# Performance work log

Hardware: AMD Instinct MI355X
Metric: run time of the kernel (lower is better)

Reference implementation:

```python
import jax, jax.numpy as jnp
import numpy as np

# Static cluster layout: B graphs, PER atoms each; first NIN are 'inside'
# (aux_ind==0), remaining NOUT are 'outside' periodic images (aux_ind==1).
B, PER, NIN, K = 256, 1024, 256, 32
NOUT = PER - NIN
N = B * PER
R = 6.0        # cutoff radius (Angstrom)
BOX = 32.0     # box side -> ~30 neighbors within R at this density


def setup_inputs() -> dict:
    key = jax.random.key(0)
    pos = jax.random.uniform(key, (N, 3), dtype=jnp.float32) * BOX
    batch = (jnp.arange(N, dtype=jnp.int32) // PER)
    aux_ind = ((jnp.arange(N, dtype=jnp.int32) % PER) >= NIN).astype(jnp.int32)
    return {"pos": pos, "batch": batch, "aux_ind": aux_ind}


def _select_neighbors(d, valid, k):
    """Pick up to k valid candidates per target, lowest candidate index first.
    d: [..., C] distances, valid: [..., C] bool. Returns (idx, mask, dist),
    each [..., k]; padded slots have mask=False and dist=0."""
    C = d.shape[-1]
    order_key = jnp.where(valid, jnp.arange(C, dtype=jnp.int32), C + 1)
    idx = jnp.argsort(order_key, axis=-1)[..., :k]          # [..., k]
    mask = jnp.take_along_axis(valid, idx, axis=-1)
    dist = jnp.where(mask, jnp.take_along_axis(d, idx, axis=-1), 0.0)
    return idx.astype(jnp.int32), mask, dist


def reference(pos, batch, aux_ind):
    # batch/aux_ind are encoded by the static contiguous layout above;
    # they parameterize the same structure torch builds via scatter_add/cumsum.
    pg = pos.reshape(B, PER, 3)
    ins = pg[:, :NIN]            # [B, NIN, 3]  inside (target + intra-conv) nodes
    outs = pg[:, NIN:]           # [B, NOUT, 3] outside (inter-conv) nodes

    # intra edges: inside -> inside, same graph, no self loops
    d_ii = jnp.sqrt(jnp.sum((ins[:, :, None, :] - ins[:, None, :, :]) ** 2, -1))  # [B,NIN,NIN]
    valid_ii = (d_ii < R) & ~jnp.eye(NIN, dtype=bool)
    idx_ii, m_ii, dist_ii = _select_neighbors(d_ii, valid_ii, K)

    # inter edges: outside -> inside, same graph
    d_io = jnp.sqrt(jnp.sum((ins[:, :, None, :] - outs[:, None, :, :]) ** 2, -1))  # [B,NIN,NOUT]
    valid_io = d_io < R
    idx_io, m_io, dist_io = _select_neighbors(d_io, valid_io, K)

    # relabel to global node indices (flow='source_to_target': row=source, col=target)
    goff = (jnp.arange(B, dtype=jnp.int32) * PER)[:, None, None]       # [B,1,1]
    tgt = jnp.broadcast_to(goff + jnp.arange(NIN, dtype=jnp.int32)[None, :, None],
                           (B, NIN, K))
    src_ii = goff + idx_ii
    src_io = goff + NIN + idx_io

    edge_index = jnp.stack([src_ii.reshape(-1), tgt.reshape(-1)], 0)        # [2, B*NIN*K]
    edge_index_inter = jnp.stack([src_io.reshape(-1), tgt.reshape(-1)], 0)  # [2, B*NIN*K]

    return (edge_index, m_ii.reshape(-1), dist_ii,
            edge_index_inter, m_io.reshape(-1), dist_io)
```

## Files before the change

### kernel.cpp

```cpp
#include <hip/hip_runtime.h>


constexpr int KK = 32;
constexpr unsigned EE = 2097152u;

typedef float v2f __attribute__((ext_vector_type(2)));

__device__ __forceinline__ v2f pk_add(v2f a, v2f b) {
    v2f d; asm("v_pk_add_f32 %0, %1, %2" : "=v"(d) : "v"(a), "v"(b)); return d;
}
__device__ __forceinline__ v2f pk_mul(v2f a, v2f b) {
    v2f d; asm("v_pk_mul_f32 %0, %1, %2" : "=v"(d) : "v"(a), "v"(b)); return d;
}

__device__ __forceinline__ int prefix_lt(unsigned long long m) {
    return __builtin_amdgcn_mbcnt_hi((unsigned)(m >> 32),
           __builtin_amdgcn_mbcnt_lo((unsigned)m, 0u));
}

__global__ __launch_bounds__(256) void mo3e_kernel(const float* __restrict__ pos,
                                                   float* __restrict__ out) {
    __shared__ float sq[3072];
    __shared__ int   slotrow[4][128];

    const int blk = blockIdx.x;
    const int b   = blk >> 6;
    const int tid = threadIdx.x;
    const int w   = tid >> 6;
    const int l   = tid & 63;
    const int i   = __builtin_amdgcn_readfirstlane(((blk & 63) << 2) | w);

    {
        const float4* g4 = (const float4*)(pos + (size_t)b * 3072);
        float4* s4 = (float4*)sq;
        s4[tid      ] = g4[tid      ];
        s4[tid + 256] = g4[tid + 256];
        s4[tid + 512] = g4[tid + 512];
    }
    __syncthreads();

    const float xi = sq[3 * i], yi = sq[3 * i + 1], zi = sq[3 * i + 2];
    const v2f nx = {-xi, -xi}, ny = {-yi, -yi}, nz = {-zi, -zi};

    int* __restrict__ row = slotrow[w];
    const int dump = 64 + l;

    unsigned long long msk[16];
    int cii = 0, cio = 0;
    int av = 3 * l;

#pragma unroll
    for (int it = 0; it < 2; ++it) {
        const float xa = sq[av], ya = sq[av + 1], za = sq[av + 2];
        const float xb = sq[av + 192], yb = sq[av + 193], zb = sq[av + 194];
        av += 384;
        const v2f qx = {xa, xb}, qy = {ya, yb}, qz = {za, zb};
        const v2f dx = pk_add(qx, nx), dy = pk_add(qy, ny), dz = pk_add(qz, nz);
        const v2f d2 = pk_add(pk_add(pk_mul(dx, dx), pk_mul(dy, dy)), pk_mul(dz, dz));
        const int c0 = it * 128;
        {
            const bool va = (d2.x < 36.0f) & ((c0 + l) != i);
            const unsigned long long m = __ballot(va);
            msk[2 * it] = m;
            int ent = cii + prefix_lt(m);
            ent = ent < 127 ? ent : 127;
            ent = va ? ent : dump;
            row[ent] = c0 + l;
            cii += __popcll(m);
        }
        {
            const bool vb = (d2.y < 36.0f) & ((c0 + 64 + l) != i);
            const unsigned long long m = __ballot(vb);
            msk[2 * it + 1] = m;
            int ent = cii + prefix_lt(m);
            ent = ent < 127 ? ent : 127;
            ent = vb ? ent : dump;
            row[ent] = c0 + 64 + l;
            cii += __popcll(m);
        }
    }
    const int S0ii = cii < KK ? cii : KK;
    if (cii < KK) {
        int pc = cii;
#pragma unroll
        for (int g = 0; g < 4; ++g) {
            const unsigned long long inv = ~msk[g];
            const bool pm = (inv >> l) & 1ull;
            int ent = pc + prefix_lt(inv);
            ent = pm ? ent : dump;
            row[ent] = g * 64 + l;
            pc += __popcll(inv);
            if (pc >= KK) break;
        }
    }

#pragma unroll
    for (int it = 2; it < 8; ++it) {
        const float xa = sq[av], ya = sq[av + 1], za = sq[av + 2];
        const float xb = sq[av + 192], yb = sq[av + 193], zb = sq[av + 194];
        av += 384;
        const v2f qx = {xa, xb}, qy = {ya, yb}, qz = {za, zb};
        const v2f dx = pk_add(qx, nx), dy = pk_add(qy, ny), dz = pk_add(qz, nz);
        const v2f d2 = pk_add(pk_add(pk_mul(dx, dx), pk_mul(dy, dy)), pk_mul(dz, dz));
        const int c0 = it * 128;
        {
            const bool va = (d2.x < 36.0f);
            const unsigned long long m = __ballot(va);
            msk[2 * it] = m;
            int ent = cio + prefix_lt(m);
            ent = ent < 95 ? ent : 95;
            ent = va ? ent + KK : dump;
            row[ent] = c0 + l;
            cio += __popcll(m);
        }
        {
            const bool vb = (d2.y < 36.0f);
            const unsigned long long m = __ballot(vb);
            msk[2 * it + 1] = m;
            int ent = cio + prefix_lt(m);
            ent = ent < 95 ? ent : 95;
            ent = vb ? ent + KK : dump;
            row[ent] = c0 + 64 + l;
            cio += __popcll(m);
        }
    }
    const int S0io = cio < KK ? cio : KK;
    if (cio < KK) {
        int pc = cio;
#pragma unroll
        for (int g = 4; g < 16; ++g) {
            const unsigned long long inv = ~msk[g];
            const bool pm = (inv >> l) & 1ull;
            int ent = pc + prefix_lt(inv);
            ent = pm ? ent + KK : dump;
            row[ent] = g * 64 + l;
            pc += __popcll(inv);
            if (pc >= KK) break;
        }
    }

    {
        const int idx = row[l];
        const float qx = sq[3 * idx], qy = sq[3 * idx + 1], qz = sq[3 * idx + 2];
        const float ddx = xi - qx, ddy = yi - qy, ddz = zi - qz;
        const float d2e = ddx * ddx + ddy * ddy + ddz * ddz;

        const bool isA = l < KK;
        const int  S0  = isA ? S0ii : S0io;
        const bool mv  = (l & 31) < S0;
        const float dist = mv ? __builtin_amdgcn_sqrtf(d2e) : 0.0f;

        const int goff = b * 1024;
        const unsigned e0  = (unsigned)(b * 256 + i) * 32u;
        const unsigned off = (isA ? 0u : 4u * EE - 32u) + e0 + (unsigned)l;

        out[off]           = (float)(goff + idx);
        out[off + EE]      = (float)(goff + i);
        out[off + 2u * EE] = mv ? 1.0f : 0.0f;
        out[off + 3u * EE] = dist;
    }
}

extern "C" void kernel_launch(void* const* d_in, const int* in_sizes, int n_in,
                              void* d_out, int out_size, void* d_ws, size_t ws_size,
                              hipStream_t stream) {
    const float* pos = (const float*)d_in[0];
    float* out = (float*)d_out;

    mo3e_kernel<<<dim3(256 * 64), dim3(256), 0, stream>>>(pos, out);
}
```

Measured before the change: 102.0 us.

## Process two target atoms per wavefront to reuse candidate loads and halve blocks

Each wavefront now handles two target atoms, so the candidate coordinates read from shared memory, and the per-graph staging of positions into LDS, are shared across two targets. The launch is halved to 8192 blocks, which halves how often each graph's positions are reloaded from global memory. The padding fill is reduced to the first 64-candidate group only, relying on at most 32 slots needing fill. The change adds register pressure and serial ballot work per wave in exchange for fewer blocks.

```diff
diff --git a/kernel.cpp b/kernel.cpp
--- a/kernel.cpp
+++ b/kernel.cpp
@@ -21,14 +21,14 @@
 __global__ __launch_bounds__(256) void mo3e_kernel(const float* __restrict__ pos,
                                                    float* __restrict__ out) {
     __shared__ float sq[3072];
-    __shared__ int   slotrow[4][128];
+    __shared__ int   slotrow[4][2][128];
 
     const int blk = blockIdx.x;
-    const int b   = blk >> 6;
+    const int b   = blk >> 5;
     const int tid = threadIdx.x;
     const int w   = tid >> 6;
     const int l   = tid & 63;
-    const int i   = __builtin_amdgcn_readfirstlane(((blk & 63) << 2) | w);
+    const int i0  = __builtin_amdgcn_readfirstlane(((blk & 31) << 3) | (w << 1));
 
     {
         const float4* g4 = (const float4*)(pos + (size_t)b * 3072);
@@ -39,123 +39,91 @@
     }
     __syncthreads();
 
-    const float xi = sq[3 * i], yi = sq[3 * i + 1], zi = sq[3 * i + 2];
-    const v2f nx = {-xi, -xi}, ny = {-yi, -yi}, nz = {-zi, -zi};
+    const float x0 = sq[3 * i0],     y0 = sq[3 * i0 + 1], z0 = sq[3 * i0 + 2];
+    const float x1 = sq[3 * i0 + 3], y1 = sq[3 * i0 + 4], z1 = sq[3 * i0 + 5];
+    const v2f nx[2] = {{-x0, -x0}, {-x1, -x1}};
+    const v2f ny[2] = {{-y0, -y0}, {-y1, -y1}};
+    const v2f nz[2] = {{-z0, -z0}, {-z1, -z1}};
 
-    int* __restrict__ row = slotrow[w];
+    int* const rows[2] = { slotrow[w][0], slotrow[w][1] };
     const int dump = 64 + l;
+    const int gs   = i0 >> 6;
 
-    unsigned long long msk[16];
-    int cii = 0, cio = 0;
+    unsigned long long m0ii[2], m0io[2];
+    int cii[2] = {0, 0}, cio[2] = {0, 0};
+
     int av = 3 * l;
-
 #pragma unroll
-    for (int it = 0; it < 2; ++it) {
+    for (int it = 0; it < 8; ++it) {
         const float xa = sq[av], ya = sq[av + 1], za = sq[av + 2];
         const float xb = sq[av + 192], yb = sq[av + 193], zb = sq[av + 194];
         av += 384;
         const v2f qx = {xa, xb}, qy = {ya, yb}, qz = {za, zb};
-        const v2f dx = pk_add(qx, nx), dy = pk_add(qy, ny), dz = pk_add(qz, nz);
-        const v2f d2 = pk_add(pk_add(pk_mul(dx, dx), pk_mul(dy, dy)), pk_mul(dz, dz));
-        const int c0 = it * 128;
-        {
-            const bool va = (d2.x < 36.0f) & ((c0 + l) != i);
-            const unsigned long long m = __ballot(va);
-            msk[2 * it] = m;
-            int ent = cii + prefix_lt(m);
-            ent = ent < 127 ? ent : 127;
-            ent = va ? ent : dump;
-            row[ent] = c0 + l;
-            cii += __popcll(m);
-        }
-        {
-            const bool vb = (d2.y < 36.0f) & ((c0 + 64 + l) != i);
-            const unsigned long long m = __ballot(vb);
-            msk[2 * it + 1] = m;
-            int ent = cii + prefix_lt(m);
-            ent = ent < 127 ? ent : 127;
-            ent = vb ? ent : dump;
-            row[ent] = c0 + 64 + l;
-            cii += __popcll(m);
-        }
-    }
-    const int S0ii = cii < KK ? cii : KK;
-    if (cii < KK) {
-        int pc = cii;
 #pragma unroll
-        for (int g = 0; g < 4; ++g) {
-            const unsigned long long inv = ~msk[g];
-            const bool pm = (inv >> l) & 1ull;
-            int ent = pc + prefix_lt(inv);
-            ent = pm ? ent : dump;
-            row[ent] = g * 64 + l;
-            pc += __popcll(inv);
-            if (pc >= KK) break;
+        for (int T = 0; T < 2; ++T) {
+            const v2f dx = pk_add(qx, nx[T]), dy = pk_add(qy, ny[T]), dz = pk_add(qz, nz[T]);
+            const v2f d2 = pk_add(pk_add(pk_mul(dx, dx), pk_mul(dy, dy)), pk_mul(dz, dz));
+#pragma unroll
+            for (int h = 0; h < 2; ++h) {
+                const int g = 2 * it + h;
+                const float dh = h ? d2.y : d2.x;
+                unsigned long long ms = __ballot(dh < 36.0f);
+                if (g < 4 && g == gs) ms &= ~(1ull << ((i0 & 63) + T));
+                const bool mine = (ms >> l) & 1ull;
+                if (g < 4) {
+                    const int e = cii[T] + prefix_lt(ms);
+                    const bool wr = mine && (e < KK);
+                    rows[T][wr ? e : dump] = (g << 6) + l;
+                    cii[T] += (int)__popcll(ms);
+                    if (g == 0) m0ii[T] = ms;
+                } else {
+                    const int e = cio[T] + prefix_lt(ms);
+                    const bool wr = mine && (e < KK);
+                    rows[T][wr ? e + KK : dump] = (g << 6) + l;
+                    cio[T] += (int)__popcll(ms);
+                    if (g == 4) m0io[T] = ms;
+                }
+            }
         }
     }
 
 #pragma unroll
-    for (int it = 2; it < 8; ++it) {
-        const float xa = sq[av], ya = sq[av + 1], za = sq[av + 2];
-        const float xb = sq[av + 192], yb = sq[av + 193], zb = sq[av + 194];
-        av += 384;
-        const v2f qx = {xa, xb}, qy = {ya, yb}, qz = {za, zb};
-        const v2f dx = pk_add(qx, nx), dy = pk_add(qy, ny), dz = pk_add(qz, nz);
-        const v2f d2 = pk_add(pk_add(pk_mul(dx, dx), pk_mul(dy, dy)), pk_mul(dz, dz));
-        const int c0 = it * 128;
-        {
-            const bool va = (d2.x < 36.0f);
-            const unsigned long long m = __ballot(va);
-            msk[2 * it] = m;
-            int ent = cio + prefix_lt(m);
-            ent = ent < 95 ? ent : 95;
-            ent = va ? ent + KK : dump;
-            row[ent] = c0 + l;
-            cio += __popcll(m);
+    for (int T = 0; T < 2; ++T) {
+        if (cii[T] < KK) {
+            const unsigned long long inv = ~m0ii[T];
+            const int e = cii[T] + prefix_lt(inv);
+            const bool wr = ((inv >> l) & 1ull) && (e < KK);
+            rows[T][wr ? e : dump] = l;
         }
-        {
-            const bool vb = (d2.y < 36.0f);
-            const unsigned long long m = __ballot(vb);
-            msk[2 * it + 1] = m;
-            int ent = cio + prefix_lt(m);
-            ent = ent < 95 ? ent : 95;
-            ent = vb ? ent + KK : dump;
-            row[ent] = c0 + 64 + l;
-            cio += __popcll(m);
-        }
-    }
-    const int S0io = cio < KK ? cio : KK;
-    if (cio < KK) {
-        int pc = cio;
-#pragma unroll
-        for (int g = 4; g < 16; ++g) {
-            const unsigned long long inv = ~msk[g];
-            const bool pm = (inv >> l) & 1ull;
-            int ent = pc + prefix_lt(inv);
-            ent = pm ? ent + KK : dump;
-            row[ent] = g * 64 + l;
-            pc += __popcll(inv);
-            if (pc >= KK) break;
+        if (cio[T] < KK) {
+            const unsigned long long inv = ~m0io[T];
+            const int e = cio[T] + prefix_lt(inv);
+            const bool wr = ((inv >> l) & 1ull) && (e < KK);
+            rows[T][wr ? e + KK : dump] = 256 + l;
         }
     }
 
-    {
-        const int idx = row[l];
+    const int goff = b << 10;
+#pragma unroll
+    for (int T = 0; T < 2; ++T) {
+        const int idx = rows[T][l];
         const float qx = sq[3 * idx], qy = sq[3 * idx + 1], qz = sq[3 * idx + 2];
+        const float xi = T ? x1 : x0, yi = T ? y1 : y0, zi = T ? z1 : z0;
         const float ddx = xi - qx, ddy = yi - qy, ddz = zi - qz;
         const float d2e = ddx * ddx + ddy * ddy + ddz * ddz;
 
         const bool isA = l < KK;
-        const int  S0  = isA ? S0ii : S0io;
+        const int  Sa  = cii[T] < KK ? cii[T] : KK;
+        const int  Sb  = cio[T] < KK ? cio[T] : KK;
+        const int  S0  = isA ? Sa : Sb;
         const bool mv  = (l & 31) < S0;
         const float dist = mv ? __builtin_amdgcn_sqrtf(d2e) : 0.0f;
 
-        const int goff = b * 1024;
-        const unsigned e0  = (unsigned)(b * 256 + i) * 32u;
+        const unsigned e0  = (unsigned)((b << 8) + i0 + T) << 5;
         const unsigned off = (isA ? 0u : 4u * EE - 32u) + e0 + (unsigned)l;
 
         out[off]           = (float)(goff + idx);
-        out[off + EE]      = (float)(goff + i);
+        out[off + EE]      = (float)(goff + i0 + T);
         out[off + 2u * EE] = mv ? 1.0f : 0.0f;
         out[off + 3u * EE] = dist;
     }
@@ -167,5 +135,5 @@
     const float* pos = (const float*)d_in[0];
     float* out = (float*)d_out;
 
-    mo3e_kernel<<<dim3(256 * 64), dim3(256), 0, stream>>>(pos, out);
+    mo3e_kernel<<<dim3(8192), dim3(256), 0, stream>>>(pos, out);
 }
```

New measurement: 103.8 us. About the same (+1.8%).
